# Performance work log

Measured on AMD Instinct MI355X. Metric: run time of the kernel, lower is better.

## Reference

```python
import jax, jax.numpy as jnp
import numpy as np

D = 512      # d_model
H = 8        # n_heads
DK = D // H  # head dim
F = 2048     # d_ff
K = 31       # depthwise kernel size
B = 8
T = 1024
LN_EPS = 1e-5
BN_EPS = 1e-5


def setup_inputs() -> dict:
    key = jax.random.key(0)
    ks = jax.random.split(key, 24)
    def nrm(k, shape, scale=0.02):
        return jax.random.normal(k, shape, jnp.float32) * scale
    d = {
        'x': jax.random.normal(ks[0], (B, T, D), jnp.float32),
        # FF1
        'ff1_ln_g': jnp.ones((D,), jnp.float32), 'ff1_ln_b': jnp.zeros((D,), jnp.float32),
        'ff1_w1': nrm(ks[1], (D, F)), 'ff1_b1': jnp.zeros((F,), jnp.float32),
        'ff1_w2': nrm(ks[2], (F, D)), 'ff1_b2': jnp.zeros((D,), jnp.float32),
        # Attention
        'attn_ln_g': jnp.ones((D,), jnp.float32), 'attn_ln_b': jnp.zeros((D,), jnp.float32),
        'wq': nrm(ks[3], (D, D)), 'bq': jnp.zeros((D,), jnp.float32),
        'wk': nrm(ks[4], (D, D)), 'bk': jnp.zeros((D,), jnp.float32),
        'wv': nrm(ks[5], (D, D)), 'bv': jnp.zeros((D,), jnp.float32),
        'wo': nrm(ks[6], (D, D)), 'bo': jnp.zeros((D,), jnp.float32),
        # Conv module
        'conv_ln_g': jnp.ones((D,), jnp.float32), 'conv_ln_b': jnp.zeros((D,), jnp.float32),
        'pw1_w': nrm(ks[7], (D, 2 * D)), 'pw1_b': jnp.zeros((2 * D,), jnp.float32),
        'dw_w': nrm(ks[8], (D, K)), 'dw_b': jnp.zeros((D,), jnp.float32),
        'bn_g': jnp.ones((D,), jnp.float32), 'bn_b': jnp.zeros((D,), jnp.float32),
        'bn_mean': jnp.zeros((D,), jnp.float32), 'bn_var': jnp.ones((D,), jnp.float32),
        'pw2_w': nrm(ks[9], (D, D)), 'pw2_b': jnp.zeros((D,), jnp.float32),
        # FF2
        'ff2_ln_g': jnp.ones((D,), jnp.float32), 'ff2_ln_b': jnp.zeros((D,), jnp.float32),
        'ff2_w1': nrm(ks[10], (D, F)), 'ff2_b1': jnp.zeros((F,), jnp.float32),
        'ff2_w2': nrm(ks[11], (F, D)), 'ff2_b2': jnp.zeros((D,), jnp.float32),
        # Final norm
        'final_ln_g': jnp.ones((D,), jnp.float32), 'final_ln_b': jnp.zeros((D,), jnp.float32),
    }
    return d


def _ln(x, g, b):
    m = jnp.mean(x, axis=-1, keepdims=True)
    v = jnp.mean(jnp.square(x - m), axis=-1, keepdims=True)
    return (x - m) * jax.lax.rsqrt(v + LN_EPS) * g + b


def _swish(x):
    return x * jax.nn.sigmoid(x)


def _ffn(x, g, b, w1, b1, w2, b2):
    h = _swish(_ln(x, g, b) @ w1 + b1)
    return h @ w2 + b2


def _block(x, ff1_ln_g, ff1_ln_b, ff1_w1, ff1_b1, ff1_w2, ff1_b2,
           attn_ln_g, attn_ln_b, wq, bq, wk, bk, wv, bv, wo, bo,
           conv_ln_g, conv_ln_b, pw1_w, pw1_b, dw_w, dw_b,
           bn_g, bn_b, bn_mean, bn_var, pw2_w, pw2_b,
           ff2_ln_g, ff2_ln_b, ff2_w1, ff2_b1, ff2_w2, ff2_b2,
           final_ln_g, final_ln_b):
    # FF1 half-residual
    x = x + 0.5 * _ffn(x, ff1_ln_g, ff1_ln_b, ff1_w1, ff1_b1, ff1_w2, ff1_b2)

    # Multi-head self-attention (mask=None)
    y = _ln(x, attn_ln_g, attn_ln_b)
    q = (y @ wq + bq).reshape(B, T, H, DK)
    k = (y @ wk + bk).reshape(B, T, H, DK)
    v = (y @ wv + bv).reshape(B, T, H, DK)
    scores = jnp.einsum('bqhd,bkhd->bhqk', q, k) / np.sqrt(DK).astype(np.float32)
    attn = jax.nn.softmax(scores, axis=-1)
    o = jnp.einsum('bhqk,bkhd->bqhd', attn, v).reshape(B, T, D)
    x = x + (o @ wo + bo)

    # Convolution module: LN -> pw1 -> GLU -> depthwise -> BN(eval) -> Swish -> pw2
    y = _ln(x, conv_ln_g, conv_ln_b)
    y = y @ pw1_w + pw1_b                      # [B,T,2D]
    a, g = y[..., :D], y[..., D:]
    y = a * jax.nn.sigmoid(g)                  # GLU over channels
    yt = jnp.transpose(y, (0, 2, 1))           # [B,D,T]
    yt = jax.lax.conv_general_dilated(
        yt, dw_w[:, None, :],                  # kernel [D,1,K]
        window_strides=(1,), padding=[(K // 2, K // 2)],
        feature_group_count=D,
        dimension_numbers=('NCH', 'OIH', 'NCH')) + dw_b[None, :, None]
    yt = (yt - bn_mean[None, :, None]) * jax.lax.rsqrt(bn_var + BN_EPS)[None, :, None]
    yt = yt * bn_g[None, :, None] + bn_b[None, :, None]
    yt = _swish(yt)
    y = jnp.transpose(yt, (0, 2, 1)) @ pw2_w + pw2_b
    x = x + y

    # FF2 half-residual
    x = x + 0.5 * _ffn(x, ff2_ln_g, ff2_ln_b, ff2_w1, ff2_b1, ff2_w2, ff2_b2)
    return _ln(x, final_ln_g, final_ln_b)


def reference(x, ff1_ln_g, ff1_ln_b, ff1_w1, ff1_b1, ff1_w2, ff1_b2,
              attn_ln_g, attn_ln_b, wq, bq, wk, bk, wv, bv, wo, bo,
              conv_ln_g, conv_ln_b, pw1_w, pw1_b, dw_w, dw_b,
              bn_g, bn_b, bn_mean, bn_var, pw2_w, pw2_b,
              ff2_ln_g, ff2_ln_b, ff2_w1, ff2_b1, ff2_w2, ff2_b2,
              final_ln_g, final_ln_b):
    return _block(x, ff1_ln_g, ff1_ln_b, ff1_w1, ff1_b1, ff1_w2, ff1_b2,
                  attn_ln_g, attn_ln_b, wq, bq, wk, bk, wv, bv, wo, bo,
                  conv_ln_g, conv_ln_b, pw1_w, pw1_b, dw_w, dw_b,
                  bn_g, bn_b, bn_mean, bn_var, pw2_w, pw2_b,
                  ff2_ln_g, ff2_ln_b, ff2_w1, ff2_b1, ff2_w2, ff2_b2,
                  final_ln_g, final_ln_b)
```

## Files before the change

kernel.cpp:

```cpp
#include <hip/hip_runtime.h>
#include <cstdint>
#include <cstddef>


typedef __attribute__((ext_vector_type(8))) short bf16x8;
typedef __attribute__((ext_vector_type(4))) float f32x4;
typedef unsigned short u16;

#define DEV static __device__ __forceinline__

DEV float bf2f(u16 u) { union { unsigned int i; float f; } x; x.i = ((unsigned int)u) << 16; return x.f; }
DEV u16 f2bf(float f) {
    union { float f; unsigned int i; } x; x.f = f;
    unsigned int r = x.i + 0x7fffu + ((x.i >> 16) & 1u);
    return (u16)(r >> 16);
}
DEV float sigm(float x) { return 1.f / (1.f + __expf(-x)); }
DEV unsigned cvt_pk_bf16(float lo, float hi) {
    unsigned r;
    asm("v_cvt_pk_bf16_f32 %0, %1, %2" : "=v"(r) : "v"(lo), "v"(hi));
    return r;
}

#define GLL16(GP, LP) __builtin_amdgcn_global_load_lds( \
    (__attribute__((address_space(1))) void*)(GP),      \
    (__attribute__((address_space(3))) void*)(LP), 16, 0, 0)

DEV const bf16x8* lds_rd(const u16* buf, int r, int s) {
    return (const bf16x8*)((const char*)buf + r * 64 + ((s ^ ((r >> 1) & 3)) << 4));
}

template <int F32IN>
DEV void ld8(const void* p, size_t off, float* v) {
    if constexpr (F32IN) {
        *(float4*)(v) = *(const float4*)((const float*)p + off);
        *(float4*)(v + 4) = *(const float4*)((const float*)p + off + 4);
    } else {
        const bf16x8 u = *(const bf16x8*)((const u16*)p + off);
#pragma unroll
        for (int j = 0; j < 8; j++) v[j] = bf2f((u16)u[j]);
    }
}

struct CastJob { const float* in; u16* out; int K, M, tile0; };
struct CastJobs { CastJob j[11]; };

__global__ __launch_bounds__(256) void k_castall(CastJobs J) {
    __shared__ float t[32][33];
    int ji = 0;
    const int bid = blockIdx.x;
    while (bid >= J.j[ji + 1].tile0) ++ji;
    const CastJob job = J.j[ji];
    const int tIdx = bid - job.tile0;
    const int tilesX = job.M >> 5;
    const int m0 = (tIdx % tilesX) * 32, k0 = (tIdx / tilesX) * 32;
    const int lx = threadIdx.x, ly = threadIdx.y;
#pragma unroll
    for (int i = 0; i < 4; i++) {
        const int kk = ly + i * 8;
        t[kk][lx] = job.in[(size_t)(k0 + kk) * job.M + m0 + lx];
    }
    __syncthreads();
#pragma unroll
    for (int i = 0; i < 4; i++) {
        const int mm = ly + i * 8;
        job.out[(size_t)(m0 + mm) * job.K + k0 + lx] = f2bf(t[lx][mm]);
    }
}

template <int INF32>
__global__ __launch_bounds__(256) void k_ln(const void* __restrict__ x,
                                            const float* __restrict__ g,
                                            const float* __restrict__ bt,
                                            u16* __restrict__ out) {
    const int row = blockIdx.x * 4 + (threadIdx.x >> 6);
    const int l = threadIdx.x & 63;
    const size_t base = (size_t)row * 512 + l * 8;
    float v[8];
    ld8<INF32>(x, base, v);
    float s = 0.f;
#pragma unroll
    for (int j = 0; j < 8; j++) s += v[j];
#pragma unroll
    for (int m = 1; m < 64; m <<= 1) s += __shfl_xor(s, m);
    const float mean = s * (1.f / 512.f);
    float ss = 0.f;
#pragma unroll
    for (int j = 0; j < 8; j++) { v[j] -= mean; ss += v[j] * v[j]; }
#pragma unroll
    for (int m = 1; m < 64; m <<= 1) ss += __shfl_xor(ss, m);
    const float rs = rsqrtf(ss * (1.f / 512.f) + 1e-5f);
    float gv[8], bv[8];
    *(float4*)(gv) = *(const float4*)(g + l * 8);
    *(float4*)(gv + 4) = *(const float4*)(g + l * 8 + 4);
    *(float4*)(bv) = *(const float4*)(bt + l * 8);
    *(float4*)(bv + 4) = *(const float4*)(bt + l * 8 + 4);
    union { u16 u[8]; bf16x8 v8; } o;
#pragma unroll
    for (int j = 0; j < 8; j++) o.u[j] = f2bf(v[j] * rs * gv[j] + bv[j]);
    *(bf16x8*)(out + base) = o.v8;
}

template <int MODE, int RESF32>
__global__ __launch_bounds__(256) void k_mergeln(const u16* __restrict__ p,
                                                 const void* __restrict__ resid,
                                                 const float* __restrict__ bias,
                                                 const float scale,
                                                 const float* __restrict__ g,
                                                 const float* __restrict__ bt,
                                                 u16* __restrict__ xout,
                                                 void* __restrict__ lnout) {
    const int row = blockIdx.x * 4 + (threadIdx.x >> 6);
    const int l = threadIdx.x & 63;
    const size_t base = (size_t)row * 512 + l * 8;
    float p0[8], p1[8], rv[8], bv[8], v[8];
    ld8<0>(p, base, p0);
    ld8<0>(p + 4194304, base, p1);
    ld8<RESF32>(resid, base, rv);
    *(float4*)(bv) = *(const float4*)(bias + l * 8);
    *(float4*)(bv + 4) = *(const float4*)(bias + l * 8 + 4);
#pragma unroll
    for (int j = 0; j < 8; j++) v[j] = rv[j] + scale * (p0[j] + p1[j] + bv[j]);
    if constexpr (MODE == 0) {
        union { u16 u[8]; bf16x8 v8; } xo;
#pragma unroll
        for (int j = 0; j < 8; j++) xo.u[j] = f2bf(v[j]);
        *(bf16x8*)(xout + base) = xo.v8;
    }
    float s = 0.f;
#pragma unroll
    for (int j = 0; j < 8; j++) s += v[j];
#pragma unroll
    for (int m = 1; m < 64; m <<= 1) s += __shfl_xor(s, m);
    const float mean = s * (1.f / 512.f);
    float ss = 0.f;
#pragma unroll
    for (int j = 0; j < 8; j++) { v[j] -= mean; ss += v[j] * v[j]; }
#pragma unroll
    for (int m = 1; m < 64; m <<= 1) ss += __shfl_xor(ss, m);
    const float rs = rsqrtf(ss * (1.f / 512.f) + 1e-5f);
    float gv[8], btv[8];
    *(float4*)(gv) = *(const float4*)(g + l * 8);
    *(float4*)(gv + 4) = *(const float4*)(g + l * 8 + 4);
    *(float4*)(btv) = *(const float4*)(bt + l * 8);
    *(float4*)(btv + 4) = *(const float4*)(bt + l * 8 + 4);
    if constexpr (MODE == 1) {
        float o[8];
#pragma unroll
        for (int j = 0; j < 8; j++) o[j] = v[j] * rs * gv[j] + btv[j];
        float* op = (float*)lnout + base;
        *(float4*)(op) = *(float4*)(o);
        *(float4*)(op + 4) = *(float4*)(o + 4);
    } else {
        union { u16 u[8]; bf16x8 v8; } o;
#pragma unroll
        for (int j = 0; j < 8; j++) o.u[j] = f2bf(v[j] * rs * gv[j] + btv[j]);
        *(bf16x8*)((u16*)lnout + base) = o.v8;
    }
}

template <int EP, int BN, int NBUF = 3, int WAVES = 4, int MINW = 1>
__global__ __launch_bounds__(WAVES * 64, MINW) void k_gemm(const u16* __restrict__ A,
                                              const u16* __restrict__ Bt,
                                              const int Kstr, const int kcount,
                                              const int M,
                                              const float* __restrict__ bias,
                                              const void* __restrict__ resid,
                                              const float scale,
                                              void* __restrict__ outp,
                                              const float* __restrict__ bias2,
                                              const float* __restrict__ bias3) {
    constexpr int CPW = BN / (WAVES / 2);
    constexpr int NI = CPW / 16;
    constexpr int ACH = 8 / WAVES ? 8 / WAVES : 1;
    constexpr int BCH = (BN / 16) / WAVES;
    constexpr int LPW = ACH + BCH;
    __shared__ __align__(16) u16 sA[NBUF][128 * 32];
    __shared__ __align__(16) u16 sB[NBUF][BN * 32];
    const int tid = threadIdx.x, w = tid >> 6, l = tid & 63;
    const int wr = (WAVES == 4 ? (w >> 1) : (w >> 2)) * 64;
    const int wc = (WAVES == 4 ? (w & 1) : (w & 3)) * CPW;
    const int bm = blockIdx.x * 128, bn = blockIdx.y * BN;
    const int kbase = (EP == 4) ? blockIdx.z * kcount : 0;
    const int l15 = l & 15, ls = l >> 4;
    const int lrow = l >> 2, lslot = l & 3;
    const int NT = kcount >> 5;
    f32x4 acc[4][NI] = {};

#define STAGE(BUF, T)                                                          \
    {                                                                          \
        _Pragma("unroll") for (int i = 0; i < ACH; i++) {                      \
            const int c = w * ACH + i;                                         \
            const int r = c * 16 + lrow;                                       \
            const int sl = lslot ^ ((r >> 1) & 3);                             \
            GLL16(A + (size_t)(bm + r) * Kstr + kbase + (T) * 32 + sl * 8,     \
                  (char*)sA[BUF] + c * 1024);                                  \
        }                                                                      \
        _Pragma("unroll") for (int i = 0; i < BCH; i++) {                      \
            const int c = w * BCH + i;                                         \
            const int r = c * 16 + lrow;                                       \
            const int sl = lslot ^ ((r >> 1) & 3);                             \
            GLL16(Bt + (size_t)(bn + r) * Kstr + kbase + (T) * 32 + sl * 8,    \
                  (char*)sB[BUF] + c * 1024);                                  \
        }                                                                      \
    }

#define WAITC(N)                                                               \
    {                                                                          \
        if constexpr (N == 2) asm volatile("s_waitcnt vmcnt(2)" ::: "memory"); \
        else if constexpr (N == 3) asm volatile("s_waitcnt vmcnt(3)" ::: "memory"); \
        else asm volatile("s_waitcnt vmcnt(4)" ::: "memory");                  \
    }

#define COMPUTE(BUF)                                                           \
    {                                                                          \
        bf16x8 af[4], bfr[NI];                                                 \
        _Pragma("unroll") for (int i = 0; i < 4; i++)                          \
            af[i] = *lds_rd(&sA[BUF][0], wr + i * 16 + l15, ls);               \
        _Pragma("unroll") for (int i = 0; i < NI; i++)                         \
            bfr[i] = *lds_rd(&sB[BUF][0], wc + i * 16 + l15, ls);              \
        __builtin_amdgcn_s_setprio(1);                                         \
        _Pragma("unroll") for (int mi = 0; mi < 4; mi++)                       \
            _Pragma("unroll") for (int ni = 0; ni < NI; ni++)                  \
                acc[mi][ni] = __builtin_amdgcn_mfma_f32_16x16x32_bf16(         \
                    af[mi], bfr[ni], acc[mi][ni], 0, 0, 0);                    \
        __builtin_amdgcn_s_setprio(0);                                         \
    }

    if constexpr (NBUF == 2) {
        STAGE(0, 0);
        int cur = 0;
        for (int t = 0; t < NT; ++t) {
            if (t + 1 < NT) {
                STAGE(cur ^ 1, t + 1);
                WAITC(LPW);
            } else {
                asm volatile("s_waitcnt vmcnt(0)" ::: "memory");
            }
            __builtin_amdgcn_s_barrier();
            __builtin_amdgcn_sched_barrier(0);
            COMPUTE(cur);
            __builtin_amdgcn_s_barrier();
            cur ^= 1;
        }
    } else {
        STAGE(0, 0);
        if (NT > 1) STAGE(1, 1);
        int cur = 0;
        for (int t = 0; t < NT; ++t) {
            if (t + 1 < NT) {
                WAITC(LPW);
            } else {
                asm volatile("s_waitcnt vmcnt(0)" ::: "memory");
            }
            __builtin_amdgcn_s_barrier();
            __builtin_amdgcn_sched_barrier(0);
            const int nxt = (cur >= 1) ? cur - 1 : cur + 2;
            if (t + 2 < NT) STAGE(nxt, t + 2);
            COMPUTE(cur);
            cur = (cur + 1 == 3) ? 0 : cur + 1;
        }
    }
#undef STAGE
#undef WAITC
#undef COMPUTE

    const bool vpath = (EP == 3) && (bn >= 1024);
    if (vpath) {
        __syncthreads();
        u16* EPB = (wc & 64) ? (u16*)sB : (u16*)sA;
#pragma unroll
        for (int ni = 0; ni < NI; ni++) {
            const int cc = (wc & 63) + ni * 16 + l15;
            const int cglob = (bn - 1024) + wc + ni * 16 + l15;
            const float b3 = bias3[cglob];
#pragma unroll
            for (int mp = 0; mp < 2; mp++) {
                unsigned pk[4];
#pragma unroll
                for (int j = 0; j < 4; j++)
                    pk[j] = cvt_pk_bf16(acc[mp * 2][ni][j] + b3, acc[mp * 2 + 1][ni][j] + b3);
                const int panel = (wr >> 5) + mp;
                const int off = (panel * 64 + ls * 16) ^ ((cc & 7) << 4);
                *(bf16x8*)((char*)EPB + cc * 256 + off) = *(bf16x8*)pk;
            }
        }
        __syncthreads();
        const int b_ = bm >> 10, tp0 = (bm & 1023) >> 5;
        u16* vout = (u16*)outp + 8388608;
        constexpr int VI = 2048 / (WAVES * 64);
#pragma unroll
        for (int i = 0; i < VI; i++) {
            const int combo = i * ((WAVES * 64) / 256) + (tid >> 8);
            const int head = combo & 1, panel = combo >> 1;
            const int t8 = tid & 255;
            const int dk = t8 >> 2, sub = t8 & 3;
            const u16* SRC = head ? (u16*)sB : (u16*)sA;
            const int off = (panel * 64 + sub * 16) ^ ((dk & 7) << 4);
            const bf16x8 vv = *(const bf16x8*)((const char*)SRC + dk * 256 + off);
            const int hg = ((bn - 1024) >> 6) + head;
            *(bf16x8*)(vout + ((size_t)(b_ * 8 + hg)) * 65536 + (size_t)(tp0 + panel) * 2048 +
                       dk * 32 + sub * 8) = vv;
        }
        return;
    }

    const int r0 = bm + wr + (l >> 4) * 4;
    const int c0 = bn + wc + l15;
#pragma unroll
    for (int mi = 0; mi < 4; mi++) {
#pragma unroll
        for (int ni = 0; ni < NI; ni++) {
            const int col = c0 + ni * 16;
#pragma unroll
            for (int j = 0; j < 4; j++) {
                const int row = r0 + mi * 16 + j;
                float v = acc[mi][ni][j];
                if constexpr (EP == 0) {
                    v += bias[col];
                    ((u16*)outp)[(size_t)row * M + col] = f2bf(v);
                } else if constexpr (EP == 1) {
                    v += bias[col];
                    v = v * sigm(v);
                    ((u16*)outp)[(size_t)row * M + col] = f2bf(v);
                } else if constexpr (EP == 2) {
                    v += bias[col];
                    const size_t idx = (size_t)row * 512 + col;
                    ((u16*)outp)[idx] = f2bf(bf2f(((const u16*)resid)[idx]) + scale * v);
                } else if constexpr (EP == 4) {
                    ((u16*)outp)[(size_t)blockIdx.z * 4194304 + (size_t)row * 512 + col] = f2bf(v);
                } else {
                    const int b_ = row >> 10, t = row & 1023;
                    u16* qb = (u16*)outp;
                    if (col < 512) {
                        const int h = col >> 6, dk = col & 63;
                        const float q = (v + bias[col]) * 0.125f;
                        qb[(size_t)(b_ * 8 + h) * 65536 + (dk >> 5) * 32768 + t * 32 + (dk & 31)] = f2bf(q);
                    } else {
                        const int c = col - 512, h = c >> 6, dk = c & 63;
                        (qb + 4194304)[(size_t)(b_ * 8 + h) * 65536 + (dk >> 5) * 32768 + t * 32 + (dk & 31)] =
                            f2bf(v + bias2[c]);
                    }
                }
            }
        }
    }
}

__global__ __launch_bounds__(512) void k_attn(const u16* __restrict__ qg,
                                              const u16* __restrict__ kg,
                                              const u16* __restrict__ vg,
                                              u16* __restrict__ og) {
    __shared__ __align__(16) u16 sK[2][4096];
    __shared__ __align__(16) u16 sV[2][4096];
    __shared__ __align__(16) char sP[8][32 * 80];
    const int tid = threadIdx.x, w = tid >> 6, l = tid & 63;
    const int bh = blockIdx.x, q0 = blockIdx.y * 128;
    const int b_ = bh >> 3, h = bh & 7;
    const int l15 = l & 15, ls = l >> 4;
    const u16* qh = qg + (size_t)bh * 65536;
    const u16* kh = kg + (size_t)bh * 65536;
    const u16* vh = vg + (size_t)bh * 65536;
    char* myP = &sP[w][0];
    bf16x8 aq[2];
#pragma unroll
    for (int kk = 0; kk < 2; kk++)
        aq[kk] = *(const bf16x8*)(qh + (size_t)kk * 32768 + (q0 + w * 16 + l15) * 32 + ls * 8);
    f32x4 oacc[4] = {};
    float lI[4] = {0.f, 0.f, 0.f, 0.f};

#define ASTAGE(BUF, KT)                                                         \
    {                                                                           \
        const int r = w * 16 + (l >> 2);                                        \
        const int sl = (l & 3) ^ ((r >> 1) & 3);                                \
        GLL16(kh + (size_t)(r >> 6) * 32768 + ((KT) * 64 + (r & 63)) * 32 + sl * 8, \
              (char*)sK[BUF] + w * 1024);                                       \
        GLL16(vh + (size_t)(KT) * 4096 + r * 32 + sl * 8, (char*)sV[BUF] + w * 1024); \
    }

    ASTAGE(0, 0);
    __syncthreads();
    int cur = 0;
    for (int kt = 0; kt < 16; kt++) {
        if (kt + 1 < 16) ASTAGE(cur ^ 1, kt + 1);
        f32x4 s[4] = {};
        __builtin_amdgcn_s_setprio(1);
#pragma unroll
        for (int kk = 0; kk < 2; kk++)
#pragma unroll
            for (int ni = 0; ni < 4; ni++) {
                const bf16x8 kb = *lds_rd(&sK[cur][0], kk * 64 + ni * 16 + l15, ls);
                s[ni] = __builtin_amdgcn_mfma_f32_16x16x32_bf16(aq[kk], kb, s[ni], 0, 0, 0);
            }
        __builtin_amdgcn_s_setprio(0);
#pragma unroll
        for (int ni = 0; ni < 4; ni++)
#pragma unroll
            for (int j = 0; j < 4; j++) {
                const float p = __expf(s[ni][j]);
                s[ni][j] = p;
                lI[j] += p;
            }
#pragma unroll
        for (int kp = 0; kp < 2; kp++)
#pragma unroll
            for (int j = 0; j < 4; j++) {
                const unsigned pk = cvt_pk_bf16(s[kp * 2][j], s[kp * 2 + 1][j]);
                *(unsigned*)(myP + (kp * 16 + ls * 4 + j) * 80 + l15 * 4) = pk;
            }
        __builtin_amdgcn_s_setprio(1);
#pragma unroll
        for (int kp = 0; kp < 2; kp++) {
            const bf16x8 pa = *(const bf16x8*)(myP + (kp * 16 + l15) * 80 + ls * 16);
#pragma unroll
            for (int no = 0; no < 4; no++) {
                const bf16x8 vb = *lds_rd(&sV[cur][0], kp * 64 + no * 16 + l15, ls);
                oacc[no] = __builtin_amdgcn_mfma_f32_16x16x32_bf16(pa, vb, oacc[no], 0, 0, 0);
            }
        }
        __builtin_amdgcn_s_setprio(0);
        __syncthreads();
        cur ^= 1;
    }
#undef ASTAGE
    float rl[4];
#pragma unroll
    for (int j = 0; j < 4; j++) {
        float lt = lI[j];
        lt += __shfl_xor(lt, 1);
        lt += __shfl_xor(lt, 2);
        lt += __shfl_xor(lt, 4);
        lt += __shfl_xor(lt, 8);
        rl[j] = 1.f / lt;
    }
#pragma unroll
    for (int no = 0; no < 4; no++)
#pragma unroll
        for (int j = 0; j < 4; j++) {
            const int t = q0 + w * 16 + ls * 4 + j;
            og[((size_t)b_ * 1024 + t) * 512 + h * 64 + no * 16 + l15] = f2bf(oacc[no][j] * rl[j]);
        }
}

__global__ __launch_bounds__(256) void k_dwconv(const u16* __restrict__ yg,
                                                const float* __restrict__ w,
                                                const float* __restrict__ wb,
                                                const float* __restrict__ bng,
                                                const float* __restrict__ bnb,
                                                const float* __restrict__ bnm,
                                                const float* __restrict__ bnv,
                                                u16* __restrict__ out) {
    __shared__ float tile[158][64];
    __shared__ float wlds[31][64];
    const int b = blockIdx.x, t0 = blockIdx.y * 128, d0 = blockIdx.z * 64;
    const int tid = threadIdx.x;
    for (int s = tid; s < 31 * 64; s += 256) {
        const int k = s >> 6, c = s & 63;
        wlds[k][c] = w[(d0 + c) * 31 + k];
    }
    for (int s = tid; s < 158 * 8; s += 256) {
        const int rr = s >> 3, c8 = s & 7;
        const int t = t0 - 15 + rr;
        float v[8];
        if ((unsigned)t < 1024u) {
            const bf16x8 va = *(const bf16x8*)(yg + ((size_t)b * 1024 + t) * 1024 + d0 + c8 * 8);
            const bf16x8 vg = *(const bf16x8*)(yg + ((size_t)b * 1024 + t) * 1024 + 512 + d0 + c8 * 8);
#pragma unroll
            for (int j = 0; j < 8; j++)
                v[j] = bf2f((u16)va[j]) * sigm(bf2f((u16)vg[j]));
        } else {
#pragma unroll
            for (int j = 0; j < 8; j++) v[j] = 0.f;
        }
        const int cs = ((c8 + (rr >> 1)) & 7) * 8;
        *(float4*)&tile[rr][cs] = *(float4*)v;
        *(float4*)&tile[rr][cs + 4] = *(float4*)(v + 4);
    }
    __syncthreads();
    const int dgrp = tid & 7;
    const int tseg = tid >> 3;
    float acc[4][8] = {};
    for (int k = 0; k < 31; k++) {
        float wv[8];
        *(float4*)wv = *(float4*)&wlds[k][dgrp * 8];
        *(float4*)(wv + 4) = *(float4*)&wlds[k][dgrp * 8 + 4];
#pragma unroll
        for (int j = 0; j < 4; j++) {
            const int row = tseg * 4 + j + k;
            const int cs = ((dgrp + (row >> 1)) & 7) * 8;
            float xv[8];
            *(float4*)xv = *(float4*)&tile[row][cs];
            *(float4*)(xv + 4) = *(float4*)&tile[row][cs + 4];
#pragma unroll
            for (int c = 0; c < 8; c++) acc[j][c] += xv[c] * wv[c];
        }
    }
    const int d = d0 + dgrp * 8;
    float scl[8], shf[8];
#pragma unroll
    for (int c = 0; c < 8; c++) {
        scl[c] = bng[d + c] * rsqrtf(bnv[d + c] + 1e-5f);
        shf[c] = bnb[d + c] + (wb[d + c] - bnm[d + c]) * scl[c];
    }
#pragma unroll
    for (int j = 0; j < 4; j++) {
        const int t = t0 + tseg * 4 + j;
        union { u16 u[8]; bf16x8 v8; } o;
#pragma unroll
        for (int c = 0; c < 8; c++) {
            float v = acc[j][c] * scl[c] + shf[c];
            o.u[c] = f2bf(v * sigm(v));
        }
        *(bf16x8*)(out + ((size_t)b * 1024 + t) * 512 + d) = o.v8;
    }
}

extern "C" void kernel_launch(void* const* d_in, const int* in_sizes, int n_in,
                              void* d_out, int out_size, void* d_ws, size_t ws_size,
                              hipStream_t stream) {
    (void)in_sizes; (void)n_in; (void)out_size; (void)ws_size;
    const float* x         = (const float*)d_in[0];
    const float* ff1_ln_g  = (const float*)d_in[1];
    const float* ff1_ln_b  = (const float*)d_in[2];
    const float* ff1_w1    = (const float*)d_in[3];
    const float* ff1_b1    = (const float*)d_in[4];
    const float* ff1_w2    = (const float*)d_in[5];
    const float* ff1_b2    = (const float*)d_in[6];
    const float* attn_ln_g = (const float*)d_in[7];
    const float* attn_ln_b = (const float*)d_in[8];
    const float* wq        = (const float*)d_in[9];
    const float* bq        = (const float*)d_in[10];
    const float* wk        = (const float*)d_in[11];
    const float* bk        = (const float*)d_in[12];
    const float* wv        = (const float*)d_in[13];
    const float* bv        = (const float*)d_in[14];
    const float* wo        = (const float*)d_in[15];
    const float* bo        = (const float*)d_in[16];
    const float* conv_ln_g = (const float*)d_in[17];
    const float* conv_ln_b = (const float*)d_in[18];
    const float* pw1_w     = (const float*)d_in[19];
    const float* pw1_b     = (const float*)d_in[20];
    const float* dw_w      = (const float*)d_in[21];
    const float* dw_b      = (const float*)d_in[22];
    const float* bn_g      = (const float*)d_in[23];
    const float* bn_b      = (const float*)d_in[24];
    const float* bn_mean   = (const float*)d_in[25];
    const float* bn_var    = (const float*)d_in[26];
    const float* pw2_w     = (const float*)d_in[27];
    const float* pw2_b     = (const float*)d_in[28];
    const float* ff2_ln_g  = (const float*)d_in[29];
    const float* ff2_ln_b  = (const float*)d_in[30];
    const float* ff2_w1    = (const float*)d_in[31];
    const float* ff2_b1    = (const float*)d_in[32];
    const float* ff2_w2    = (const float*)d_in[33];
    const float* ff2_b2    = (const float*)d_in[34];
    const float* fin_ln_g  = (const float*)d_in[35];
    const float* fin_ln_b  = (const float*)d_in[36];

    char* wsb = (char*)d_ws;
    u16*  W_ff1w1 = (u16*)(wsb + ((size_t)0 << 20));
    u16*  W_ff1w2 = (u16*)(wsb + ((size_t)2 << 20));
    u16*  W_qkv   = (u16*)(wsb + ((size_t)4 << 20));
    u16*  W_wo    = (u16*)(wsb + ((size_t)6 << 20));
    u16*  W_pw1   = (u16*)(wsb + ((size_t)7 << 20));
    u16*  W_pw2   = (u16*)(wsb + ((size_t)8 << 20));
    u16*  W_ff2w1 = (u16*)(wsb + ((size_t)9 << 20));
    u16*  W_ff2w2 = (u16*)(wsb + ((size_t)11 << 20));
    u16*   xcur   = (u16*)(wsb + ((size_t)13 << 20));
    u16*  actA    = (u16*)(wsb + ((size_t)29 << 20));
    u16*  actB    = (u16*)(wsb + ((size_t)37 << 20));
    u16*  PART    = (u16*)(wsb + ((size_t)70 << 20));

    CastJobs J;
    auto setj = [&](int i, const float* in, u16* out, int K, int M) {
        J.j[i].in = in; J.j[i].out = out; J.j[i].K = K; J.j[i].M = M;
    };
    setj(0, ff1_w1, W_ff1w1, 512, 2048);
    setj(1, ff1_w2, W_ff1w2, 2048, 512);
    setj(2, wq, W_qkv,          512, 512);
    setj(3, wk, W_qkv + 262144, 512, 512);
    setj(4, wv, W_qkv + 524288, 512, 512);
    setj(5, wo, W_wo, 512, 512);
    setj(6, pw1_w, W_pw1, 512, 1024);
    setj(7, pw2_w, W_pw2, 512, 512);
    setj(8, ff2_w1, W_ff2w1, 512, 2048);
    setj(9, ff2_w2, W_ff2w2, 2048, 512);
    int tot = 0;
    for (int i = 0; i < 10; i++) {
        J.j[i].tile0 = tot;
        tot += (J.j[i].M >> 5) * (J.j[i].K >> 5);
    }
    J.j[10].tile0 = tot;
    k_castall<<<tot, dim3(32, 8), 0, stream>>>(J);

    k_ln<1><<<2048, 256, 0, stream>>>(x, ff1_ln_g, ff1_ln_b, actA);
    k_gemm<1, 128, 2, 8><<<dim3(64, 16), 512, 0, stream>>>(actA, W_ff1w1, 512, 512, 2048, ff1_b1, nullptr, 0.f, actB, nullptr, nullptr);
    k_gemm<4, 128, 3, 8, 6><<<dim3(64, 4, 2), 512, 0, stream>>>(actB, W_ff1w2, 2048, 1024, 512, nullptr, nullptr, 0.f, PART, nullptr, nullptr);
    k_mergeln<0, 1><<<2048, 256, 0, stream>>>(PART, x, ff1_b2, 0.5f, attn_ln_g, attn_ln_b, xcur, actA);
    k_gemm<3, 128, 3, 8, 6><<<dim3(64, 12), 512, 0, stream>>>(actA, W_qkv, 512, 512, 1536, bq, nullptr, 0.f, actB, bk, bv);
    k_attn<<<dim3(64, 8), 512, 0, stream>>>(actB, actB + 4194304, actB + 8388608, actA);
    k_gemm<4, 128, 3, 8, 6><<<dim3(64, 4, 2), 512, 0, stream>>>(actA, W_wo, 512, 256, 512, nullptr, nullptr, 0.f, PART, nullptr, nullptr);
    k_mergeln<0, 0><<<2048, 256, 0, stream>>>(PART, xcur, bo, 1.f, conv_ln_g, conv_ln_b, xcur, actA);
    k_gemm<0, 128, 3, 8, 6><<<dim3(64, 8), 512, 0, stream>>>(actA, W_pw1, 512, 512, 1024, pw1_b, nullptr, 0.f, actB, nullptr, nullptr);
    k_dwconv<<<dim3(8, 8, 8), 256, 0, stream>>>(actB, dw_w, dw_b, bn_g, bn_b, bn_mean, bn_var, actA);
    k_gemm<4, 128, 3, 8, 6><<<dim3(64, 4, 2), 512, 0, stream>>>(actA, W_pw2, 512, 256, 512, nullptr, nullptr, 0.f, PART, nullptr, nullptr);
    k_mergeln<0, 0><<<2048, 256, 0, stream>>>(PART, xcur, pw2_b, 1.f, ff2_ln_g, ff2_ln_b, xcur, actA);
    k_gemm<1, 128, 2, 8><<<dim3(64, 16), 512, 0, stream>>>(actA, W_ff2w1, 512, 512, 2048, ff2_b1, nullptr, 0.f, actB, nullptr, nullptr);
    k_gemm<4, 128, 3, 8, 6><<<dim3(64, 4, 2), 512, 0, stream>>>(actB, W_ff2w2, 2048, 1024, 512, nullptr, nullptr, 0.f, PART, nullptr, nullptr);
    k_mergeln<1, 0><<<2048, 256, 0, stream>>>(PART, xcur, ff2_b2, 0.5f, fin_ln_g, fin_ln_b, nullptr, d_out);
}
```

Baseline: 269.2 us.

## Fuse GLU into pw1 GEMM epilogue and merge first LayerNorm into cast kernel

The pw1 weight columns are interleaved during the cast so each GEMM wave holds matching value and gate columns. The GLU (a*sigmoid(g)) is then applied in a new GEMM epilogue that writes a half-width bf16 output, and the depthwise conv reads that output directly. Separately, the initial FF1 LayerNorm is folded into the weight-cast launch as extra blocks, removing one kernel launch. This cuts intermediate traffic and launch overhead, at the cost of scalar, uncoalesced 2-byte stores in the new epilogue.

```diff
diff --git a/kernel.cpp b/kernel.cpp
--- a/kernel.cpp
+++ b/kernel.cpp
@@ -42,13 +42,46 @@
     }
 }
 
-struct CastJob { const float* in; u16* out; int K, M, tile0; };
-struct CastJobs { CastJob j[11]; };
+struct CastJob { const float* in; u16* out; int K, M, tile0, rmp; };
+struct CastJobs {
+    CastJob j[11];
+    const float* lnx; const float* lng; const float* lnb; u16* lnout;
+};
 
 __global__ __launch_bounds__(256) void k_castall(CastJobs J) {
     __shared__ float t[32][33];
+    const int bid = blockIdx.x;
+    const int tid = threadIdx.y * 32 + threadIdx.x;
+    if (bid >= J.j[10].tile0) {
+        const int row = (bid - J.j[10].tile0) * 4 + (tid >> 6);
+        const int l = tid & 63;
+        const size_t base = (size_t)row * 512 + l * 8;
+        float v[8];
+        ld8<1>(J.lnx, base, v);
+        float s = 0.f;
+#pragma unroll
+        for (int j = 0; j < 8; j++) s += v[j];
+#pragma unroll
+        for (int m = 1; m < 64; m <<= 1) s += __shfl_xor(s, m);
+        const float mean = s * (1.f / 512.f);
+        float ss = 0.f;
+#pragma unroll
+        for (int j = 0; j < 8; j++) { v[j] -= mean; ss += v[j] * v[j]; }
+#pragma unroll
+        for (int m = 1; m < 64; m <<= 1) ss += __shfl_xor(ss, m);
+        const float rs = rsqrtf(ss * (1.f / 512.f) + 1e-5f);
+        float gv[8], bv[8];
+        *(float4*)(gv) = *(const float4*)(J.lng + l * 8);
+        *(float4*)(gv + 4) = *(const float4*)(J.lng + l * 8 + 4);
+        *(float4*)(bv) = *(const float4*)(J.lnb + l * 8);
+        *(float4*)(bv + 4) = *(const float4*)(J.lnb + l * 8 + 4);
+        union { u16 u[8]; bf16x8 v8; } o;
+#pragma unroll
+        for (int j = 0; j < 8; j++) o.u[j] = f2bf(v[j] * rs * gv[j] + bv[j]);
+        *(bf16x8*)(J.lnout + base) = o.v8;
+        return;
+    }
     int ji = 0;
-    const int bid = blockIdx.x;
     while (bid >= J.j[ji + 1].tile0) ++ji;
     const CastJob job = J.j[ji];
     const int tIdx = bid - job.tile0;
@@ -64,41 +97,10 @@
 #pragma unroll
     for (int i = 0; i < 4; i++) {
         const int mm = ly + i * 8;
-        job.out[(size_t)(m0 + mm) * job.K + k0 + lx] = f2bf(t[lx][mm]);
-    }
-}
-
-template <int INF32>
-__global__ __launch_bounds__(256) void k_ln(const void* __restrict__ x,
-                                            const float* __restrict__ g,
-                                            const float* __restrict__ bt,
-                                            u16* __restrict__ out) {
-    const int row = blockIdx.x * 4 + (threadIdx.x >> 6);
-    const int l = threadIdx.x & 63;
-    const size_t base = (size_t)row * 512 + l * 8;
-    float v[8];
-    ld8<INF32>(x, base, v);
-    float s = 0.f;
-#pragma unroll
-    for (int j = 0; j < 8; j++) s += v[j];
-#pragma unroll
-    for (int m = 1; m < 64; m <<= 1) s += __shfl_xor(s, m);
-    const float mean = s * (1.f / 512.f);
-    float ss = 0.f;
-#pragma unroll
-    for (int j = 0; j < 8; j++) { v[j] -= mean; ss += v[j] * v[j]; }
-#pragma unroll
-    for (int m = 1; m < 64; m <<= 1) ss += __shfl_xor(ss, m);
-    const float rs = rsqrtf(ss * (1.f / 512.f) + 1e-5f);
-    float gv[8], bv[8];
-    *(float4*)(gv) = *(const float4*)(g + l * 8);
-    *(float4*)(gv + 4) = *(const float4*)(g + l * 8 + 4);
-    *(float4*)(bv) = *(const float4*)(bt + l * 8);
-    *(float4*)(bv + 4) = *(const float4*)(bt + l * 8 + 4);
-    union { u16 u[8]; bf16x8 v8; } o;
-#pragma unroll
-    for (int j = 0; j < 8; j++) o.u[j] = f2bf(v[j] * rs * gv[j] + bv[j]);
-    *(bf16x8*)(out + base) = o.v8;
+        const int m = m0 + mm;
+        const int mr = job.rmp ? ((((m & 511) >> 4) << 5) + ((m >> 9) << 4) + (m & 15)) : m;
+        job.out[(size_t)mr * job.K + k0 + lx] = f2bf(t[lx][mm]);
+    }
 }
 
 template <int MODE, int RESF32>
@@ -264,6 +266,22 @@
 #undef STAGE
 #undef WAITC
 #undef COMPUTE
+
+    if constexpr (EP == 5) {
+        const int creal = ((bn + wc) >> 1) + l15;
+        const float ba = bias[creal], bg = bias[creal + 512];
+        const int r0e = bm + wr + ls * 4;
+#pragma unroll
+        for (int mi = 0; mi < 4; mi++)
+#pragma unroll
+            for (int j = 0; j < 4; j++) {
+                const int row = r0e + mi * 16 + j;
+                const float a = acc[mi][0][j] + ba;
+                const float g = acc[mi][1][j] + bg;
+                ((u16*)outp)[(size_t)row * 512 + creal] = f2bf(a * sigm(g));
+            }
+        return;
+    }
 
     const bool vpath = (EP == 3) && (bn >= 1024);
     if (vpath) {
@@ -463,11 +481,9 @@
         const int t = t0 - 15 + rr;
         float v[8];
         if ((unsigned)t < 1024u) {
-            const bf16x8 va = *(const bf16x8*)(yg + ((size_t)b * 1024 + t) * 1024 + d0 + c8 * 8);
-            const bf16x8 vg = *(const bf16x8*)(yg + ((size_t)b * 1024 + t) * 1024 + 512 + d0 + c8 * 8);
-#pragma unroll
-            for (int j = 0; j < 8; j++)
-                v[j] = bf2f((u16)va[j]) * sigm(bf2f((u16)vg[j]));
+            const bf16x8 va = *(const bf16x8*)(yg + ((size_t)b * 1024 + t) * 512 + d0 + c8 * 8);
+#pragma unroll
+            for (int j = 0; j < 8; j++) v[j] = bf2f((u16)va[j]);
         } else {
 #pragma unroll
             for (int j = 0; j < 8; j++) v[j] = 0.f;
@@ -572,8 +588,8 @@
     u16*  PART    = (u16*)(wsb + ((size_t)70 << 20));
 
     CastJobs J;
-    auto setj = [&](int i, const float* in, u16* out, int K, int M) {
-        J.j[i].in = in; J.j[i].out = out; J.j[i].K = K; J.j[i].M = M;
+    auto setj = [&](int i, const float* in, u16* out, int K, int M, int rmp = 0) {
+        J.j[i].in = in; J.j[i].out = out; J.j[i].K = K; J.j[i].M = M; J.j[i].rmp = rmp;
     };
     setj(0, ff1_w1, W_ff1w1, 512, 2048);
     setj(1, ff1_w2, W_ff1w2, 2048, 512);
@@ -581,7 +597,7 @@
     setj(3, wk, W_qkv + 262144, 512, 512);
     setj(4, wv, W_qkv + 524288, 512, 512);
     setj(5, wo, W_wo, 512, 512);
-    setj(6, pw1_w, W_pw1, 512, 1024);
+    setj(6, pw1_w, W_pw1, 512, 1024, 1);
     setj(7, pw2_w, W_pw2, 512, 512);
     setj(8, ff2_w1, W_ff2w1, 512, 2048);
     setj(9, ff2_w2, W_ff2w2, 2048, 512);
@@ -591,9 +607,9 @@
         tot += (J.j[i].M >> 5) * (J.j[i].K >> 5);
     }
     J.j[10].tile0 = tot;
-    k_castall<<<tot, dim3(32, 8), 0, stream>>>(J);
-
-    k_ln<1><<<2048, 256, 0, stream>>>(x, ff1_ln_g, ff1_ln_b, actA);
+    J.lnx = x; J.lng = ff1_ln_g; J.lnb = ff1_ln_b; J.lnout = actA;
+    k_castall<<<tot + 2048, dim3(32, 8), 0, stream>>>(J);
+
     k_gemm<1, 128, 2, 8><<<dim3(64, 16), 512, 0, stream>>>(actA, W_ff1w1, 512, 512, 2048, ff1_b1, nullptr, 0.f, actB, nullptr, nullptr);
     k_gemm<4, 128, 3, 8, 6><<<dim3(64, 4, 2), 512, 0, stream>>>(actB, W_ff1w2, 2048, 1024, 512, nullptr, nullptr, 0.f, PART, nullptr, nullptr);
     k_mergeln<0, 1><<<2048, 256, 0, stream>>>(PART, x, ff1_b2, 0.5f, attn_ln_g, attn_ln_b, xcur, actA);
@@ -601,7 +617,7 @@
     k_attn<<<dim3(64, 8), 512, 0, stream>>>(actB, actB + 4194304, actB + 8388608, actA);
     k_gemm<4, 128, 3, 8, 6><<<dim3(64, 4, 2), 512, 0, stream>>>(actA, W_wo, 512, 256, 512, nullptr, nullptr, 0.f, PART, nullptr, nullptr);
     k_mergeln<0, 0><<<2048, 256, 0, stream>>>(PART, xcur, bo, 1.f, conv_ln_g, conv_ln_b, xcur, actA);
-    k_gemm<0, 128, 3, 8, 6><<<dim3(64, 8), 512, 0, stream>>>(actA, W_pw1, 512, 512, 1024, pw1_b, nullptr, 0.f, actB, nullptr, nullptr);
+    k_gemm<5, 128, 3, 8, 6><<<dim3(64, 8), 512, 0, stream>>>(actA, W_pw1, 512, 512, 512, pw1_b, nullptr, 0.f, actB, nullptr, nullptr);
     k_dwconv<<<dim3(8, 8, 8), 256, 0, stream>>>(actB, dw_w, dw_b, bn_g, bn_b, bn_mean, bn_var, actA);
     k_gemm<4, 128, 3, 8, 6><<<dim3(64, 4, 2), 512, 0, stream>>>(actA, W_pw2, 512, 256, 512, nullptr, nullptr, 0.f, PART, nullptr, nullptr);
     k_mergeln<0, 0><<<2048, 256, 0, stream>>>(PART, xcur, pw2_b, 1.f, ff2_ln_g, ff2_ln_b, xcur, actA);
```

Result: no change. 266.1 us (-1.2%).
